# Kernel optimization log

Hardware: AMD Instinct MI355X
Metric: run time of the kernel (lower is better)

Reference implementation:

```python
import jax, jax.numpy as jnp
import numpy as np

S, D, H, HD, FF = 4096, 1024, 16, 64, 4096  # seq, d_embed, heads, head_dim, hidden
EPS = 1e-6  # flax LayerNorm default epsilon


def layer_norm(x, scale, bias):
    mu = jnp.mean(x, axis=-1, keepdims=True)
    var = jnp.var(x, axis=-1, keepdims=True)
    return (x - mu) * jax.lax.rsqrt(var + EPS) * scale + bias


def rope(x):
    # x: [S, H, HD]; standard half-split rotary embedding, base 10000
    half = x.shape[-1] // 2
    freq = 1.0 / (10000.0 ** (jnp.arange(half, dtype=x.dtype) / half))  # [half]
    ang = jnp.arange(x.shape[0], dtype=x.dtype)[:, None] * freq          # [S, half]
    cos = jnp.cos(ang)[:, None, :]
    sin = jnp.sin(ang)[:, None, :]
    x1, x2 = x[..., :half], x[..., half:]
    return jnp.concatenate([x1 * cos - x2 * sin, x2 * cos + x1 * sin], axis=-1)


def setup_inputs() -> dict:
    key = jax.random.key(0)
    ks = jax.random.split(key, 8)
    s = 0.02
    return {
        "x": jax.random.normal(ks[0], (S, D), jnp.float32),
        "ln1_scale": jnp.ones((D,), jnp.float32), "ln1_bias": jnp.zeros((D,), jnp.float32),
        "ln2_scale": jnp.ones((D,), jnp.float32), "ln2_bias": jnp.zeros((D,), jnp.float32),
        "Wq": jax.random.normal(ks[1], (D, H, HD), jnp.float32) * s, "bq": jnp.zeros((H, HD), jnp.float32),
        "Wk": jax.random.normal(ks[2], (D, H, HD), jnp.float32) * s, "bk": jnp.zeros((H, HD), jnp.float32),
        "Wv": jax.random.normal(ks[3], (D, H, HD), jnp.float32) * s, "bv": jnp.zeros((H, HD), jnp.float32),
        "Wo": jax.random.normal(ks[4], (H, HD, D), jnp.float32) * s, "bo": jnp.zeros((D,), jnp.float32),
        "W1": jax.random.normal(ks[5], (D, FF), jnp.float32) * s, "b1": jnp.zeros((FF,), jnp.float32),
        "W2": jax.random.normal(ks[6], (FF, D), jnp.float32) * s, "b2": jnp.zeros((D,), jnp.float32),
    }


def reference(x, ln1_scale, ln1_bias, ln2_scale, ln2_bias, Wq, bq, Wk, bk, Wv, bv, Wo, bo, W1, b1, W2, b2):
    # Pre-LN attention block with RoPE fused into QK scores
    y = layer_norm(x, ln1_scale, ln1_bias)
    q = jnp.einsum('sd,dhc->shc', y, Wq) + bq  # [S,H,HD]
    k = jnp.einsum('sd,dhc->shc', y, Wk) + bk
    v = jnp.einsum('sd,dhc->shc', y, Wv) + bv
    q = rope(q)
    k = rope(k)
    scores = jnp.einsum('qhc,khc->hqk', q, k) / jnp.sqrt(jnp.asarray(HD, x.dtype))  # [H,S,S]
    p = jax.nn.softmax(scores, axis=-1)
    o = jnp.einsum('hqk,khc->qhc', p, v)                # [S,H,HD]
    attn_out = jnp.einsum('qhc,hcd->qd', o, Wo) + bo    # [S,D]
    x = x + attn_out
    # Pre-LN GELU MLP block
    y = layer_norm(x, ln2_scale, ln2_bias)
    y = jax.nn.gelu(y @ W1 + b1, approximate=False)
    x = x + (y @ W2 + b2)
    return x
```

## Files before the change

### kernel.cpp

```cpp
#include <hip/hip_runtime.h>
#include <hip/hip_bf16.h>
#include <math.h>

using bf16 = __hip_bfloat16;
typedef __attribute__((ext_vector_type(8))) short short8;
typedef __attribute__((ext_vector_type(4))) short s16x4;
typedef __attribute__((ext_vector_type(4))) float f32x4;

constexpr int S = 4096, D = 1024, H = 16, HD = 64, FF = 4096;

static __device__ __forceinline__ float tof(bf16 v) { return __bfloat162float(v); }
static __device__ __forceinline__ bf16 tob(float v) { return __float2bfloat16(v); }
static __device__ __forceinline__ short tobs(float v) {
    bf16 h = __float2bfloat16(v);
    return *reinterpret_cast<short*>(&h);
}
static __device__ __forceinline__ unsigned pkbf16(float a, float b) {
    __hip_bfloat162 h = __float22bfloat162_rn(make_float2(a, b));
    return *reinterpret_cast<unsigned*>(&h);
}

#if __has_builtin(__builtin_amdgcn_exp2f)
#define EXP2(x) __builtin_amdgcn_exp2f(x)
#else
#define EXP2(x) exp2f(x)
#endif

static __device__ __forceinline__ f32x4 mfma16(short8 a, short8 b, f32x4 c) {
    return __builtin_amdgcn_mfma_f32_16x16x32_bf16(a, b, c, 0, 0, 0);
}
static __device__ __forceinline__ void stage16(const bf16* g, bf16* l) {
    __builtin_amdgcn_global_load_lds((__attribute__((address_space(1))) void*)g,
                                     (__attribute__((address_space(3))) void*)l, 16, 0, 0);
}
static __device__ __forceinline__ void pl32swap(unsigned& a, unsigned& b) {
    asm("v_permlane32_swap_b32 %0, %1" : "+v"(a), "+v"(b));
}
static __device__ __forceinline__ void pl16swap(unsigned& a, unsigned& b) {
    asm("v_permlane16_swap_b32 %0, %1" : "+v"(a), "+v"(b));
}

__global__ __launch_bounds__(256) void rope_tab(float2* __restrict__ tab) {
    int i = blockIdx.x * 256 + threadIdx.x;
    int s = i >> 5, dim = i & 31;
    float freq = __expf(-(float)dim * (9.210340371976184f / 32.f));
    float sn, cs;
    sincosf((float)s * freq, &sn, &cs);
    tab[i] = make_float2(cs, sn);
}

__global__ __launch_bounds__(256) void ln_kernel(const float* __restrict__ x,
                                                 const float* __restrict__ scale,
                                                 const float* __restrict__ bias,
                                                 bf16* __restrict__ y) {
    int row = blockIdx.x, t = threadIdx.x;
    const float* xr = x + (size_t)row * D;
    float v[4], s = 0.f, ss = 0.f;
#pragma unroll
    for (int i = 0; i < 4; ++i) {
        v[i] = xr[t + 256 * i];
        s += v[i]; ss += v[i] * v[i];
    }
    __shared__ float r0[256], r1[256];
    r0[t] = s; r1[t] = ss;
    __syncthreads();
    for (int off = 128; off; off >>= 1) {
        if (t < off) { r0[t] += r0[t + off]; r1[t] += r1[t + off]; }
        __syncthreads();
    }
    float mu  = r0[0] * (1.f / D);
    float var = r1[0] * (1.f / D) - mu * mu;
    float inv = rsqrtf(var + 1e-6f);
    bf16* yr = y + (size_t)row * D;
#pragma unroll
    for (int i = 0; i < 4; ++i) {
        int c = t + 256 * i;
        yr[c] = tob((v[i] - mu) * inv * scale[c] + bias[c]);
    }
}

__global__ __launch_bounds__(256) void wtrans_all(
    const float* __restrict__ Wq, const float* __restrict__ Wk,
    const float* __restrict__ Wv, const float* __restrict__ Wo,
    const float* __restrict__ W1, const float* __restrict__ W2,
    const float* __restrict__ bq, const float* __restrict__ bk,
    const float* __restrict__ bv,
    bf16* __restrict__ BTqkv, bf16* __restrict__ BTo,
    bf16* __restrict__ BT1, bf16* __restrict__ BT2, float* __restrict__ bqkv) {
    int id = blockIdx.x;
    if (id >= 12288) {
        int i = (id - 12288) * 256 + threadIdx.x;
        bqkv[i] = i < 1024 ? bq[i] : (i < 2048 ? bk[i - 1024] : bv[i - 2048]);
        return;
    }
    const float* W; bf16* dst; int K, N, local;
    if (id < 3072)      { int s = id >> 10; W = s == 0 ? Wq : (s == 1 ? Wk : Wv);
                          dst = BTqkv + (size_t)s * 1048576; K = 1024; N = 1024; local = id & 1023; }
    else if (id < 4096) { W = Wo; dst = BTo; K = 1024; N = 1024; local = id - 3072; }
    else if (id < 8192) { W = W1; dst = BT1; K = 1024; N = 4096; local = id - 4096; }
    else                { W = W2; dst = BT2; K = 4096; N = 1024; local = id - 8192; }
    int ls = (N == 4096) ? 7 : 5;
    int nt = (local & ((1 << ls) - 1)) << 5, kt = (local >> ls) << 5;
    __shared__ float t[32][33];
    int tid = threadIdx.x, r = tid >> 5, c = tid & 31;
#pragma unroll
    for (int p = 0; p < 4; ++p)
        t[r + p * 8][c] = W[(size_t)(kt + r + p * 8) * N + nt + c];
    __syncthreads();
#pragma unroll
    for (int p = 0; p < 4; ++p)
        dst[(size_t)(nt + r + p * 8) * K + kt + c] = tob(t[c][r + p * 8]);
}

#define EPI_RES  1
#define EPI_GELU 2
#define EPI_QKV  3

template <int EPI, int MT>
__global__ __launch_bounds__(256, MT == 128 ? 2 : 3) void gemm_bt(
    const bf16* __restrict__ A, const bf16* __restrict__ BT,
    const float* __restrict__ bias, const float* resid, void* out, void* out2,
    int M, int N, int K, int kLen) {
    constexpr int NJ = (MT == 128) ? 4 : 2;
    __shared__ bf16 As[2][MT * 32];
    __shared__ bf16 Bs[2][128 * 32];
    const int tid = threadIdx.x;
    const int w = tid >> 6, lane = tid & 63;
    const int quad = lane >> 4, l16 = lane & 15;
    const int rowBase = blockIdx.y * MT, colBase = blockIdx.x * 128;
    const int kStart = blockIdx.z * kLen;
    const int wr = (MT == 128) ? (w >> 1) * 64 : 0;
    const int wc = (MT == 128) ? (w & 1) * 64 : w * 32;
    const int sr = lane >> 2;
    const int skb = (((lane & 3) ^ ((lane >> 3) & 3)) * 8);
    const int fr = (l16 >> 1) & 3;
    f32x4 acc[4][NJ] = {};

    auto stage = [&](int k0, int b) {
        if constexpr (MT == 128) {
#pragma unroll
            for (int t = 0; t < 2; ++t) {
                int inst = w * 2 + t;
                int r = inst * 16 + sr;
                stage16(A  + (size_t)(rowBase + r) * K + kStart + k0 + skb, &As[b][inst * 512]);
                stage16(BT + (size_t)(colBase + r) * K + kStart + k0 + skb, &Bs[b][inst * 512]);
            }
        } else {
            stage16(A + (size_t)(rowBase + w * 16 + sr) * K + kStart + k0 + skb, &As[b][w * 512]);
#pragma unroll
            for (int t = 0; t < 2; ++t) {
                int inst = w + t * 4;
                stage16(BT + (size_t)(colBase + inst * 16 + sr) * K + kStart + k0 + skb, &Bs[b][inst * 512]);
            }
        }
    };

    stage(0, 0);
    const int nSteps = kLen >> 5;
    for (int s = 0; s < nSteps; ++s) {
        const int cb = s & 1;
        __builtin_amdgcn_s_barrier();
        if (s + 1 < nSteps) {
            stage((s + 1) << 5, cb ^ 1);
            if constexpr (MT == 128) asm volatile("s_waitcnt vmcnt(4)" ::: "memory");
            else                     asm volatile("s_waitcnt vmcnt(3)" ::: "memory");
        } else {
            asm volatile("s_waitcnt vmcnt(0)" ::: "memory");
        }
        __builtin_amdgcn_s_barrier();
        const bf16* pa = &As[cb][(wr + l16) * 32 + (quad ^ fr) * 8];
        const bf16* pb = &Bs[cb][(wc + l16) * 32 + (quad ^ fr) * 8];
        short8 a[4], b[NJ];
#pragma unroll
        for (int i = 0; i < 4; ++i) a[i] = *(const short8*)(pa + i * 512);
#pragma unroll
        for (int j = 0; j < NJ; ++j) b[j] = *(const short8*)(pb + j * 512);
#pragma unroll
        for (int i = 0; i < 4; ++i)
#pragma unroll
            for (int j = 0; j < NJ; ++j) acc[i][j] = mfma16(a[i], b[j], acc[i][j]);
    }
    if (EPI == EPI_QKV) {
        bf16* QKo = (bf16*)out;
        bf16* VTo = (bf16*)out2;
        if (colBase >= 2048) {
#pragma unroll
            for (int j = 0; j < NJ; ++j) {
                int c = colBase + wc + j * 16 + l16;
                float bj = bias[c];
                size_t cc = (size_t)(c - 2048) * 4096;
#pragma unroll
                for (int i = 0; i < 4; ++i) {
                    int r0 = rowBase + wr + i * 16 + quad * 4;
                    s16x4 ov = {tobs(acc[i][j][0] + bj), tobs(acc[i][j][1] + bj),
                                tobs(acc[i][j][2] + bj), tobs(acc[i][j][3] + bj)};
                    *(s16x4*)(VTo + cc + r0) = ov;
                }
            }
        } else {
            const bool isq = colBase < 1024;
            const float qs = isq ? 0.125f * 1.44269504088896f : 1.f;
            const float2* tab = (const float2*)resid;
#pragma unroll
            for (int j2 = 0; j2 < 2; ++j2) {
                int dim = j2 * 16 + l16;
                int c1 = colBase + wc + j2 * 16 + l16, c2 = c1 + 32;
                float b1v = bias[c1], b2v = bias[c2];
#pragma unroll
                for (int i = 0; i < 4; ++i) {
#pragma unroll
                    for (int reg = 0; reg < 4; ++reg) {
                        int s = rowBase + wr + i * 16 + quad * 4 + reg;
                        float2 t = tab[s * 32 + dim];
                        float x1 = acc[i][j2][reg] + b1v;
                        float x2 = acc[i][j2 + 2][reg] + b2v;
                        QKo[(size_t)s * 2048 + c1] = tob((x1 * t.x - x2 * t.y) * qs);
                        QKo[(size_t)s * 2048 + c2] = tob((x2 * t.x + x1 * t.y) * qs);
                    }
                }
            }
        }
    } else {
#pragma unroll
        for (int j = 0; j < NJ; ++j) {
            int c = colBase + wc + j * 16 + l16;
            float bj = bias[c];
#pragma unroll
            for (int i = 0; i < 4; ++i) {
                int r0 = rowBase + wr + i * 16 + quad * 4;
#pragma unroll
                for (int reg = 0; reg < 4; ++reg) {
                    size_t idx = (size_t)(r0 + reg) * N + c;
                    float val = acc[i][j][reg] + bj;
                    if (EPI == EPI_RES) {
                        ((float*)out)[idx] = val + resid[idx];
                    } else {
                        float g = 0.5f * val * (1.f + erff(val * 0.70710678118f));
                        ((bf16*)out)[idx] = tob(g);
                    }
                }
            }
        }
    }
}

__global__ __launch_bounds__(256, 2) void attn_kernel(const bf16* __restrict__ QK,
                                                      const bf16* __restrict__ VT,
                                                      bf16* __restrict__ o) {
    const int bx = blockIdx.x;
    const int h = bx >> 5, qb = bx & 31;
    const int w = threadIdx.x >> 6, lane = threadIdx.x & 63;
    const int quad = lane >> 4, l16 = lane & 15;
    const int q0w = qb * 128 + w * 32;
    const bf16* Qh = QK + h * 64;
    const bf16* Kh = QK + 1024 + h * 64;
    const bf16* Vh = VT + (size_t)h * 64 * 4096;

    __shared__ char smem[32768];

    const int sw = l16 & 7;
    const int rloc = lane >> 3, slot = lane & 7;
    const int schunk = (slot ^ rloc) * 8;
    const int row0 = w * 16 + rloc, row1 = w * 16 + 8 + rloc;

    short8 qf[2][2];
#pragma unroll
    for (int qt = 0; qt < 2; ++qt)
#pragma unroll
        for (int c = 0; c < 2; ++c)
            qf[qt][c] = *(const short8*)(Qh + (size_t)(q0w + qt * 16 + l16) * 2048 + c * 32 + quad * 8);

    const short ob = (l16 == 0) ? (short)0x3F80 : (short)0;
    const short8 ones8 = {ob, ob, ob, ob, ob, ob, ob, ob};

    f32x4 acc[4][2] = {};
    f32x4 accl[2] = {};
    const f32x4 zero = {0.f, 0.f, 0.f, 0.f};

    {
        bf16* Ksb = (bf16*)smem;
        bf16* Vsb = (bf16*)(smem + 8192);
        stage16(Kh + (size_t)row0 * 2048 + schunk, Ksb + w * 1024);
        stage16(Kh + (size_t)row1 * 2048 + schunk, Ksb + w * 1024 + 512);
        stage16(Vh + (size_t)row0 * 4096 + schunk, Vsb + w * 1024);
        stage16(Vh + (size_t)row1 * 4096 + schunk, Vsb + w * 1024 + 512);
    }

#pragma unroll 2
    for (int t = 0; t < 64; ++t) {
        char* curb = smem + (t & 1) * 16384;
        char* nxtb = smem + ((t + 1) & 1) * 16384;
        __builtin_amdgcn_s_barrier();
        if (t < 63) {
            const int ktA = (t + 1) * 64;
            bf16* Ksb = (bf16*)nxtb;
            bf16* Vsb = (bf16*)(nxtb + 8192);
            stage16(Kh + (size_t)(ktA + row0) * 2048 + schunk, Ksb + w * 1024);
            stage16(Kh + (size_t)(ktA + row1) * 2048 + schunk, Ksb + w * 1024 + 512);
            stage16(Vh + (size_t)row0 * 4096 + ktA + schunk, Vsb + w * 1024);
            stage16(Vh + (size_t)row1 * 4096 + ktA + schunk, Vsb + w * 1024 + 512);
            asm volatile("s_waitcnt vmcnt(4)" ::: "memory");
        } else {
            asm volatile("s_waitcnt vmcnt(0)" ::: "memory");
        }
        __builtin_amdgcn_s_barrier();

        const bf16* Ks = (const bf16*)curb;
        const bf16* Vs = (const bf16*)(curb + 8192);

        unsigned u[4][2][2];
#pragma unroll
        for (int nt = 0; nt < 4; ++nt) {
            const bf16* kr = Ks + (nt * 16 + l16) * 64;
            short8 k0 = *(const short8*)(kr + ((quad ^ sw) * 8));
            short8 k1 = *(const short8*)(kr + (((quad + 4) ^ sw) * 8));
#pragma unroll
            for (int qt = 0; qt < 2; ++qt) {
                f32x4 st = mfma16(k1, qf[qt][1], mfma16(k0, qf[qt][0], zero));
                u[nt][qt][0] = pkbf16(EXP2(st[0]), EXP2(st[1]));
                u[nt][qt][1] = pkbf16(EXP2(st[2]), EXP2(st[3]));
            }
        }
#pragma unroll
        for (int c = 0; c < 2; ++c) {
            short8 pB[2];
#pragma unroll
            for (int qt = 0; qt < 2; ++qt) {
                unsigned a0 = u[2 * c][qt][0], a1 = u[2 * c][qt][1];
                unsigned b0 = u[2 * c + 1][qt][0], b1 = u[2 * c + 1][qt][1];
                pl32swap(a0, b0);
                pl32swap(a1, b1);
                pl16swap(a0, b0);
                pl16swap(a1, b1);
                union { unsigned u4[4]; short8 s8; } pk;
                pk.u4[0] = a0; pk.u4[1] = a1; pk.u4[2] = b0; pk.u4[3] = b1;
                pB[qt] = pk.s8;
                accl[qt] = mfma16(ones8, pB[qt], accl[qt]);
            }
#pragma unroll
            for (int vt = 0; vt < 4; ++vt) {
                short8 vf = *(const short8*)(Vs + (vt * 16 + l16) * 64 + (((c * 4 + quad) ^ sw) * 8));
#pragma unroll
                for (int qt = 0; qt < 2; ++qt)
                    acc[vt][qt] = mfma16(vf, pB[qt], acc[vt][qt]);
            }
        }
    }
#pragma unroll
    for (int qt = 0; qt < 2; ++qt) {
        float lq = __shfl(accl[qt][0], l16, 64);
        float linv = 1.f / lq;
        int q = q0w + qt * 16 + l16;
#pragma unroll
        for (int vt = 0; vt < 4; ++vt) {
            s16x4 ov = {tobs(acc[vt][qt][0] * linv), tobs(acc[vt][qt][1] * linv),
                        tobs(acc[vt][qt][2] * linv), tobs(acc[vt][qt][3] * linv)};
            *(s16x4*)(o + (size_t)q * 1024 + h * 64 + vt * 16 + quad * 4) = ov;
        }
    }
}

extern "C" void kernel_launch(void* const* d_in, const int* in_sizes, int n_in,
                              void* d_out, int out_size, void* d_ws, size_t ws_size,
                              hipStream_t stream) {
    const float* x   = (const float*)d_in[0];
    const float* s1  = (const float*)d_in[1];
    const float* b1n = (const float*)d_in[2];
    const float* s2  = (const float*)d_in[3];
    const float* b2n = (const float*)d_in[4];
    const float* Wq  = (const float*)d_in[5];
    const float* bq  = (const float*)d_in[6];
    const float* Wk  = (const float*)d_in[7];
    const float* bk  = (const float*)d_in[8];
    const float* Wv  = (const float*)d_in[9];
    const float* bv  = (const float*)d_in[10];
    const float* Wo  = (const float*)d_in[11];
    const float* bo  = (const float*)d_in[12];
    const float* W1  = (const float*)d_in[13];
    const float* b1  = (const float*)d_in[14];
    const float* W2  = (const float*)d_in[15];
    const float* b2  = (const float*)d_in[16];

    char* ws = (char*)d_ws;
    bf16*  y    = (bf16*)(ws);
    bf16*  QK   = (bf16*)(ws + (8ull  << 20));
    bf16*  BTo  = (bf16*)(ws + (24ull << 20));
    float* bqkv = (float*)(ws + (27ull << 20));
    float2* tab = (float2*)(ws + (28ull << 20));
    bf16*  o    = (bf16*)(ws + (32ull << 20));
    bf16*  hb   = (bf16*)(ws + (40ull << 20));
    bf16*  BTqkv= (bf16*)(ws + (40ull << 20));
    bf16*  VT   = (bf16*)(ws + (72ull << 20));
    bf16*  BT1  = (bf16*)(ws + (80ull << 20));
    bf16*  BT2  = (bf16*)(ws + (88ull << 20));
    float* x1   = (float*)d_out;

    wtrans_all<<<12300, 256, 0, stream>>>(Wq, Wk, Wv, Wo, W1, W2, bq, bk, bv,
                                          BTqkv, BTo, BT1, BT2, bqkv);

    rope_tab<<<512, 256, 0, stream>>>(tab);

    ln_kernel<<<S, 256, 0, stream>>>(x, s1, b1n, y);

    gemm_bt<EPI_QKV, 128><<<dim3(24, 32), 256, 0, stream>>>(y, BTqkv, bqkv, (const float*)tab, QK, VT, S, 3072, D, D);

    attn_kernel<<<H * 32, 256, 0, stream>>>(QK, VT, o);

    gemm_bt<EPI_RES, 64><<<dim3(8, 64), 256, 0, stream>>>(o, BTo, bo, x, x1, nullptr, S, D, D, D);

    ln_kernel<<<S, 256, 0, stream>>>(x1, s2, b2n, y);

    gemm_bt<EPI_GELU, 128><<<dim3(32, 32), 256, 0, stream>>>(y, BT1, b1, nullptr, hb, nullptr, S, FF, D, D);

    gemm_bt<EPI_RES, 64><<<dim3(8, 64), 256, 0, stream>>>(hb, BT2, b2, x1, x1, nullptr, S, D, FF, FF);
}
```

Baseline: 416.8 us.

## Add 256x256 tiled 512-thread GEMM for QKV and FFN1 projections

Introduces a new gemm256 kernel with 256x256 output tiles, 8 waves, a K-step of 64, double-buffered LDS with XOR swizzle, and MFMA interleaved with next-tile staging plus s_setprio. The QKV (with RoPE epilogue) and W1+GELU GEMMs move to it, and the old gemm_bt drops its QKV epilogue. Larger tiles raise arithmetic intensity and cut global and LDS traffic per flop. In exchange the grid shrinks to 192 and 256 blocks, which may underfill the 256 CUs, and register pressure rises with 128 accumulator floats per thread.

```diff
diff --git a/kernel.cpp b/kernel.cpp
--- a/kernel.cpp
+++ b/kernel.cpp
@@ -115,6 +115,142 @@
 #define EPI_RES  1
 #define EPI_GELU 2
 #define EPI_QKV  3
+
+template <int EPI>
+__global__ __launch_bounds__(512, 2) void gemm256(
+    const bf16* __restrict__ A, const bf16* __restrict__ BT,
+    const float* __restrict__ bias, const float* __restrict__ tabp,
+    void* out, void* out2, int N, int K) {
+    __shared__ bf16 lds[2][2][2][8192];
+    const int tid = threadIdx.x;
+    const int w = tid >> 6, lane = tid & 63;
+    const int quad = lane >> 4, l16 = lane & 15;
+    const int wr = w >> 2, wn = w & 3;
+    const int rowBase = blockIdx.y * 256, colBase = blockIdx.x * 256;
+    const int cx = l16 & 7;
+
+    f32x4 acc[8][4] = {};
+
+    auto stageHalf = [&](int b, int mat, int h, int tk) {
+        const bf16* base = mat ? BT : A;
+        const int rb = (mat ? colBase : rowBase) + h * 128;
+#pragma unroll
+        for (int i = 0; i < 2; ++i) {
+            int s = i * 512 + tid;
+            int row = s >> 3, gch = (s & 7) ^ ((s >> 3) & 7);
+            stage16(base + (size_t)(rb + row) * K + tk * 64 + gch * 8,
+                    &lds[b][mat][h][s * 8]);
+        }
+    };
+    auto ldA = [&](int b, int mh, short8 a[4][2]) {
+#pragma unroll
+        for (int mf = 0; mf < 4; ++mf)
+#pragma unroll
+            for (int ks = 0; ks < 2; ++ks)
+                a[mf][ks] = *(const short8*)&lds[b][0][wr]
+                    [(mh * 64 + mf * 16 + l16) * 64 + (((ks * 4 + quad) ^ cx) * 8)];
+    };
+    auto ldB = [&](int b, int nh, short8 bb[2][2]) {
+#pragma unroll
+        for (int nf = 0; nf < 2; ++nf)
+#pragma unroll
+            for (int ks = 0; ks < 2; ++ks)
+                bb[nf][ks] = *(const short8*)&lds[b][1][wn >> 1]
+                    [((wn & 1) * 64 + nh * 32 + nf * 16 + l16) * 64 + (((ks * 4 + quad) ^ cx) * 8)];
+    };
+    auto domm = [&](short8 a[4][2], short8 bb[2][2], int mh, int nh) {
+        __builtin_amdgcn_s_setprio(1);
+#pragma unroll
+        for (int mf = 0; mf < 4; ++mf)
+#pragma unroll
+            for (int nf = 0; nf < 2; ++nf)
+#pragma unroll
+                for (int ks = 0; ks < 2; ++ks)
+                    acc[mh * 4 + mf][nh * 2 + nf] =
+                        mfma16(a[mf][ks], bb[nf][ks], acc[mh * 4 + mf][nh * 2 + nf]);
+        __builtin_amdgcn_s_setprio(0);
+    };
+
+    const int nT = K >> 6;
+    stageHalf(0, 0, 0, 0); stageHalf(0, 0, 1, 0);
+    stageHalf(0, 1, 0, 0); stageHalf(0, 1, 1, 0);
+    asm volatile("s_waitcnt vmcnt(0)" ::: "memory");
+    __builtin_amdgcn_s_barrier();
+
+    short8 af0[4][2], af1[4][2], bf0[2][2], bf1[2][2];
+    for (int t = 0; t < nT; ++t) {
+        const int b = t & 1;
+        ldA(b, 0, af0); ldB(b, 0, bf0);
+        if (t + 1 < nT) { stageHalf(b ^ 1, 1, 0, t + 1); stageHalf(b ^ 1, 1, 1, t + 1); }
+        domm(af0, bf0, 0, 0);
+        ldB(b, 1, bf1);
+        if (t + 1 < nT) { stageHalf(b ^ 1, 0, 0, t + 1); stageHalf(b ^ 1, 0, 1, t + 1); }
+        domm(af0, bf1, 0, 1);
+        ldA(b, 1, af1);
+        domm(af1, bf1, 1, 1);
+        domm(af1, bf0, 1, 0);
+        asm volatile("s_waitcnt vmcnt(0)" ::: "memory");
+        __builtin_amdgcn_s_barrier();
+    }
+
+    if (EPI == EPI_QKV) {
+        bf16* QKo = (bf16*)out;
+        bf16* VTo = (bf16*)out2;
+        if (colBase >= 2048) {
+#pragma unroll
+            for (int nf = 0; nf < 4; ++nf) {
+                int c = colBase + wn * 64 + nf * 16 + l16;
+                float bj = bias[c];
+                size_t cc = (size_t)(c - 2048) * 4096;
+#pragma unroll
+                for (int mf = 0; mf < 8; ++mf) {
+                    int r0 = rowBase + wr * 128 + mf * 16 + quad * 4;
+                    s16x4 ov = {tobs(acc[mf][nf][0] + bj), tobs(acc[mf][nf][1] + bj),
+                                tobs(acc[mf][nf][2] + bj), tobs(acc[mf][nf][3] + bj)};
+                    *(s16x4*)(VTo + cc + r0) = ov;
+                }
+            }
+        } else {
+            const bool isq = colBase < 1024;
+            const float qs = isq ? 0.125f * 1.44269504088896f : 1.f;
+            const float2* tab = (const float2*)tabp;
+#pragma unroll
+            for (int j2 = 0; j2 < 2; ++j2) {
+                int dim = j2 * 16 + l16;
+                int c1 = colBase + wn * 64 + j2 * 16 + l16, c2 = c1 + 32;
+                float b1v = bias[c1], b2v = bias[c2];
+#pragma unroll
+                for (int mf = 0; mf < 8; ++mf) {
+#pragma unroll
+                    for (int reg = 0; reg < 4; ++reg) {
+                        int s = rowBase + wr * 128 + mf * 16 + quad * 4 + reg;
+                        float2 tt = tab[s * 32 + dim];
+                        float x1 = acc[mf][j2][reg] + b1v;
+                        float x2 = acc[mf][j2 + 2][reg] + b2v;
+                        QKo[(size_t)s * 2048 + c1] = tob((x1 * tt.x - x2 * tt.y) * qs);
+                        QKo[(size_t)s * 2048 + c2] = tob((x2 * tt.x + x1 * tt.y) * qs);
+                    }
+                }
+            }
+        }
+    } else {
+#pragma unroll
+        for (int nf = 0; nf < 4; ++nf) {
+            int c = colBase + wn * 64 + nf * 16 + l16;
+            float bj = bias[c];
+#pragma unroll
+            for (int mf = 0; mf < 8; ++mf) {
+                int r0 = rowBase + wr * 128 + mf * 16 + quad * 4;
+#pragma unroll
+                for (int reg = 0; reg < 4; ++reg) {
+                    float val = acc[mf][nf][reg] + bj;
+                    float g = 0.5f * val * (1.f + erff(val * 0.70710678118f));
+                    ((bf16*)out)[(size_t)(r0 + reg) * N + c] = tob(g);
+                }
+            }
+        }
+    }
+}
 
 template <int EPI, int MT>
 __global__ __launch_bounds__(256, MT == 128 ? 2 : 3) void gemm_bt(
@@ -180,64 +316,22 @@
 #pragma unroll
             for (int j = 0; j < NJ; ++j) acc[i][j] = mfma16(a[i], b[j], acc[i][j]);
     }
-    if (EPI == EPI_QKV) {
-        bf16* QKo = (bf16*)out;
-        bf16* VTo = (bf16*)out2;
-        if (colBase >= 2048) {
-#pragma unroll
-            for (int j = 0; j < NJ; ++j) {
-                int c = colBase + wc + j * 16 + l16;
-                float bj = bias[c];
-                size_t cc = (size_t)(c - 2048) * 4096;
-#pragma unroll
-                for (int i = 0; i < 4; ++i) {
-                    int r0 = rowBase + wr + i * 16 + quad * 4;
-                    s16x4 ov = {tobs(acc[i][j][0] + bj), tobs(acc[i][j][1] + bj),
-                                tobs(acc[i][j][2] + bj), tobs(acc[i][j][3] + bj)};
-                    *(s16x4*)(VTo + cc + r0) = ov;
-                }
-            }
-        } else {
-            const bool isq = colBase < 1024;
-            const float qs = isq ? 0.125f * 1.44269504088896f : 1.f;
-            const float2* tab = (const float2*)resid;
-#pragma unroll
-            for (int j2 = 0; j2 < 2; ++j2) {
-                int dim = j2 * 16 + l16;
-                int c1 = colBase + wc + j2 * 16 + l16, c2 = c1 + 32;
-                float b1v = bias[c1], b2v = bias[c2];
-#pragma unroll
-                for (int i = 0; i < 4; ++i) {
-#pragma unroll
-                    for (int reg = 0; reg < 4; ++reg) {
-                        int s = rowBase + wr + i * 16 + quad * 4 + reg;
-                        float2 t = tab[s * 32 + dim];
-                        float x1 = acc[i][j2][reg] + b1v;
-                        float x2 = acc[i][j2 + 2][reg] + b2v;
-                        QKo[(size_t)s * 2048 + c1] = tob((x1 * t.x - x2 * t.y) * qs);
-                        QKo[(size_t)s * 2048 + c2] = tob((x2 * t.x + x1 * t.y) * qs);
-                    }
-                }
-            }
-        }
-    } else {
-#pragma unroll
-        for (int j = 0; j < NJ; ++j) {
-            int c = colBase + wc + j * 16 + l16;
-            float bj = bias[c];
-#pragma unroll
-            for (int i = 0; i < 4; ++i) {
-                int r0 = rowBase + wr + i * 16 + quad * 4;
-#pragma unroll
-                for (int reg = 0; reg < 4; ++reg) {
-                    size_t idx = (size_t)(r0 + reg) * N + c;
-                    float val = acc[i][j][reg] + bj;
-                    if (EPI == EPI_RES) {
-                        ((float*)out)[idx] = val + resid[idx];
-                    } else {
-                        float g = 0.5f * val * (1.f + erff(val * 0.70710678118f));
-                        ((bf16*)out)[idx] = tob(g);
-                    }
+#pragma unroll
+    for (int j = 0; j < NJ; ++j) {
+        int c = colBase + wc + j * 16 + l16;
+        float bj = bias[c];
+#pragma unroll
+        for (int i = 0; i < 4; ++i) {
+            int r0 = rowBase + wr + i * 16 + quad * 4;
+#pragma unroll
+            for (int reg = 0; reg < 4; ++reg) {
+                size_t idx = (size_t)(r0 + reg) * N + c;
+                float val = acc[i][j][reg] + bj;
+                if (EPI == EPI_RES) {
+                    ((float*)out)[idx] = val + resid[idx];
+                } else {
+                    float g = 0.5f * val * (1.f + erff(val * 0.70710678118f));
+                    ((bf16*)out)[idx] = tob(g);
                 }
             }
         }
@@ -402,7 +496,7 @@
 
     ln_kernel<<<S, 256, 0, stream>>>(x, s1, b1n, y);
 
-    gemm_bt<EPI_QKV, 128><<<dim3(24, 32), 256, 0, stream>>>(y, BTqkv, bqkv, (const float*)tab, QK, VT, S, 3072, D, D);
+    gemm256<EPI_QKV><<<dim3(12, 16), 512, 0, stream>>>(y, BTqkv, bqkv, (const float*)tab, QK, VT, 3072, D);
 
     attn_kernel<<<H * 32, 256, 0, stream>>>(QK, VT, o);
 
@@ -410,7 +504,7 @@
 
     ln_kernel<<<S, 256, 0, stream>>>(x1, s2, b2n, y);
 
-    gemm_bt<EPI_GELU, 128><<<dim3(32, 32), 256, 0, stream>>>(y, BT1, b1, nullptr, hb, nullptr, S, FF, D, D);
+    gemm256<EPI_GELU><<<dim3(16, 16), 512, 0, stream>>>(y, BT1, b1, nullptr, hb, nullptr, FF, D);
 
     gemm_bt<EPI_RES, 64><<<dim3(8, 64), 256, 0, stream>>>(hb, BT2, b2, x1, x1, nullptr, S, D, FF, FF);
 }
```

New measurement: 435.8 us. +4.6%, slower.
